# Kernel tuning notes

Hardware: AMD Instinct MI355X
Metric: run time of the kernel (lower is better)

## Reference

```python
import jax, jax.numpy as jnp
import numpy as np

N = 1024      # number of atoms
L = 64        # latent_size
VOCAB = 20    # vocab_size (len(ATOM_CATEGORIES))


def _lin(key, fan_in, fan_out):
    # mimic torch nn.Linear init: U(-1/sqrt(fan_in), 1/sqrt(fan_in))
    kw, kb = jax.random.split(key)
    s = 1.0 / np.sqrt(fan_in)
    W = jax.random.uniform(kw, (fan_in, fan_out), minval=-s, maxval=s, dtype=jnp.float32)
    b = jax.random.uniform(kb, (fan_out,), minval=-s, maxval=s, dtype=jnp.float32)
    return W, b


def setup_inputs() -> dict:
    key = jax.random.key(0)
    ks = jax.random.split(key, 9)
    We1, be1 = _lin(ks[3], 2 * L + 1, L)   # mlp_e layer 1
    We2, be2 = _lin(ks[4], L, L)           # mlp_e layer 2
    Wh1, bh1 = _lin(ks[5], L + 1, L)       # mlp_h layer 1
    Wh2, bh2 = _lin(ks[6], L, L)           # mlp_h layer 2
    Wo, bo = _lin(ks[7], L, 1)             # output_mlp
    return {
        "atom_categories": jax.random.randint(ks[0], (N,), 0, VOCAB),
        "atom_coordinates": jax.random.normal(ks[1], (N, 3), dtype=jnp.float32),
        "learnable_matrix": jax.random.normal(ks[2], (VOCAB, L), dtype=jnp.float32),
        "We1": We1, "be1": be1, "We2": We2, "be2": be2,
        "Wh1": Wh1, "bh1": bh1, "Wh2": Wh2, "bh2": bh2,
        "Wo": Wo, "bo": bo,
    }


def reference(atom_categories, atom_coordinates, learnable_matrix,
              We1, be1, We2, be2, Wh1, bh1, Wh2, bh2, Wo, bo):
    Z = atom_coordinates
    # init_H: learnable_matrix.T @ one_hot(cat) == row gather
    H = learnable_matrix[atom_categories]                       # [N, L]

    # pairwise squared distances ||Z_i - Z_j||^2
    d2 = jnp.sum((Z[:, None, :] - Z[None, :, :]) ** 2, axis=-1)  # [N, N]

    # mlp_e layer 1 on concat(H_i, H_j, d2): split We1 to avoid materializing concat
    W1i, W1j, w1z = We1[:L], We1[L:2 * L], We1[2 * L]            # [L,L],[L,L],[L]
    pre_i = H @ W1i                                              # [N, L]
    pre_j = H @ W1j                                              # [N, L]
    h1 = jnp.tanh(pre_i[:, None, :] + pre_j[None, :, :]
                  + d2[:, :, None] * w1z + be1)                  # [N, N, L]
    W_e = jnp.tanh(h1 @ We2 + be2)                               # [N, N, L]

    # V[i] = sum over j != i of sum_l W_e[i,j,l]
    total = jnp.sum(W_e, axis=(1, 2))                            # [N]
    diag = jnp.einsum('iil->i', W_e)                             # [N]
    V = total - diag                                             # [N]

    # mlp_h on concat(H_i, V_i): split Wh1
    hh = jnp.tanh(H @ Wh1[:L] + V[:, None] * Wh1[L] + bh1)       # [N, L]
    newH = jnp.tanh(hh @ Wh2 + bh2)                              # [N, L]

    Hsum = jnp.sum(newH, axis=0)                                 # [L]
    return (Hsum @ Wo + bo)[0]                                   # scalar
```

## Files before the change

kernel.cpp:

```cpp
#include <hip/hip_runtime.h>
#include <hip/hip_bf16.h>


#define N_ATOMS 1024
#define L_DIM 64
#define TPB 256
#define CSCALE 2.8853900817779268f

typedef _Float16 f16x8 __attribute__((ext_vector_type(8)));
typedef __fp16  fp16x2 __attribute__((ext_vector_type(2)));
typedef float f32x4 __attribute__((ext_vector_type(4)));

__device__ __forceinline__ float tanh_fast(float x) {
    float e = __builtin_amdgcn_exp2f(x * CSCALE);
    float r = __builtin_amdgcn_rcpf(e + 1.0f);
    return fmaf(-2.0f, r, 1.0f);
}

__global__ __launch_bounds__(256) void k_prep(const int* __restrict__ cat,
                                              const float* __restrict__ LM,
                                              const float* __restrict__ We1,
                                              const float* __restrict__ be1,
                                              const float* __restrict__ We2,
                                              const float* __restrict__ be2,
                                              float* __restrict__ H,
                                              float* __restrict__ preI,
                                              float* __restrict__ P3,
                                              f16x8* __restrict__ BHi,
                                              f16x8* __restrict__ BLo,
                                              float* __restrict__ biasPk,
                                              float* __restrict__ out) {
    int t = threadIdx.x;
    int sub = t >> 6, l = t & 63;
    if (blockIdx.x == 0 && t == 0) out[0] = 0.f;

    __shared__ float W1s[2 * L_DIM * L_DIM];
    __shared__ float hs[4][L_DIM];
#pragma unroll
    for (int p = 0; p < 2 * L_DIM * L_DIM / 256; p++)
        W1s[p * 256 + t] = We1[p * 256 + t];

    if (blockIdx.x == 0) {
        int lane = t & 63, grp = t >> 6;
        int nlo = lane & 15, quad = lane >> 4;
#pragma unroll
        for (int pp = grp * 2; pp < grp * 2 + 2; pp++) {
            int nt = pp >> 1, kt = pp & 1;
            f16x8 hi8, lo8;
#pragma unroll
            for (int e = 0; e < 8; e++) {
                float x = We2[(kt * 32 + quad * 8 + e) * L_DIM + nt * 16 + nlo];
                float wp = -2.0f * CSCALE * x;
                _Float16 hi = (_Float16)wp;
                hi8[e] = hi;
                lo8[e] = (_Float16)(wp - (float)hi);
            }
            BHi[pp * 64 + lane] = hi8;
            BLo[pp * 64 + lane] = lo8;
        }
        if (t < 64) {
            float cs = 0.f;
            for (int m = 0; m < L_DIM; m++) cs += We2[m * L_DIM + t];
            biasPk[t] = CSCALE * (be2[t] + cs);
        }
    }

    float bl = be1[l];
    for (int g = 0; g < 4; g++) {
        int i = blockIdx.x * 16 + g * 4 + sub;
        __syncthreads();
        float hv = LM[cat[i] * L_DIM + l];
        hs[sub][l] = hv;
        H[i * L_DIM + l] = hv;
        __syncthreads();
        float s1 = 0.f, s2 = 0.f;
#pragma unroll
        for (int m = 0; m < L_DIM; m++) {
            float h = hs[sub][m];
            s1 = fmaf(h, W1s[m * L_DIM + l], s1);
            s2 = fmaf(h, W1s[(L_DIM + m) * L_DIM + l], s2);
        }
        preI[i * L_DIM + l] = s1 * CSCALE;
        int cc = i >> 4;
        int Ll = i & 15;
        int quad = (l >> 3) & 3;
        int L = quad * 16 + Ll;
        int gg = ((l >> 5) << 1) | ((l >> 2) & 1);
        int e2 = l & 3;
        P3[cc * 1024 + gg * 256 + L * 4 + e2] = (s2 + bl) * CSCALE;
    }
}

__global__ __launch_bounds__(TPB) void k_main(const float* __restrict__ Z,
                                              const float* __restrict__ We1,
                                              const float* __restrict__ preI,
                                              const float* __restrict__ P3,
                                              const f16x8* __restrict__ BHi,
                                              const f16x8* __restrict__ BLo,
                                              const float* __restrict__ biasPk,
                                              float* __restrict__ Vpart) {
    int b = blockIdx.x;
    int i = b >> 1;
    int half = b & 1;
    int t = threadIdx.x;
    int lane = t & 63;
    int wave = t >> 6;
    int nlo = lane & 15;
    int quad = lane >> 4;

    __shared__ float d2s[512];
    __shared__ float red[TPB];
    __shared__ f16x8 bHs[8 * 64];
    __shared__ f16x8 bLs[8 * 64];

    float zi0 = Z[i * 3], zi1 = Z[i * 3 + 1], zi2 = Z[i * 3 + 2];
    for (int p = t; p < 512; p += TPB) {
        int j = half * 512 + p;
        float a = zi0 - Z[j * 3], bb = zi1 - Z[j * 3 + 1], c = zi2 - Z[j * 3 + 2];
        d2s[p] = a * a + bb * bb + c * c;
    }

    if (wave == 0) {
#pragma unroll
        for (int pp = 0; pp < 8; pp++) bHs[pp * 64 + lane] = BHi[pp * 64 + lane];
    } else if (wave == 1) {
#pragma unroll
        for (int pp = 0; pp < 8; pp++) bLs[pp * 64 + lane] = BLo[pp * 64 + lane];
    }

    f32x4 aiR[4], wzR[4];
#pragma unroll
    for (int g = 0; g < 4; g++) {
        int mb = ((g >> 1) << 5) + (quad << 3) + ((g & 1) << 2);
        aiR[g] = *(const f32x4*)(preI + i * L_DIM + mb);
        f32x4 wz = *(const f32x4*)(We1 + 2 * L_DIM * L_DIM + mb);
        wzR[g] = wz * CSCALE;
    }
    float biasR[4];
#pragma unroll
    for (int nt = 0; nt < 4; nt++) biasR[nt] = biasPk[nt * 16 + nlo];

    const float* Pbase = P3 + (half * 32 + wave * 8) * 1024 + lane * 4;

    __syncthreads();

    float Vr = 0.f;
    for (int k = 0; k < 8; k++) {
        int jl0 = (wave * 8 + k) * 16;
        float d2 = d2s[jl0 + nlo];
        const float* pb = Pbase + k * 1024;
        f32x4 p0 = *(const f32x4*)(pb + 0 * 256);
        f32x4 p1 = *(const f32x4*)(pb + 1 * 256);
        f32x4 p2 = *(const f32x4*)(pb + 2 * 256);
        f32x4 p3 = *(const f32x4*)(pb + 3 * 256);

        float h[4][4];
#pragma unroll
        for (int e2 = 0; e2 < 4; e2++) {
            {
                float z = fmaf(d2, wzR[0][e2], aiR[0][e2] + p0[e2]);
                h[0][e2] = __builtin_amdgcn_rcpf(__builtin_amdgcn_exp2f(z) + 1.0f);
            }
            {
                float z = fmaf(d2, wzR[1][e2], aiR[1][e2] + p1[e2]);
                h[1][e2] = __builtin_amdgcn_rcpf(__builtin_amdgcn_exp2f(z) + 1.0f);
            }
            {
                float z = fmaf(d2, wzR[2][e2], aiR[2][e2] + p2[e2]);
                h[2][e2] = __builtin_amdgcn_rcpf(__builtin_amdgcn_exp2f(z) + 1.0f);
            }
            {
                float z = fmaf(d2, wzR[3][e2], aiR[3][e2] + p3[e2]);
                h[3][e2] = __builtin_amdgcn_rcpf(__builtin_amdgcn_exp2f(z) + 1.0f);
            }
        }
        union { f16x8 v; fp16x2 h2[4]; } u0, u1;
        u0.h2[0] = __builtin_amdgcn_cvt_pkrtz(h[0][0], h[0][1]);
        u0.h2[1] = __builtin_amdgcn_cvt_pkrtz(h[0][2], h[0][3]);
        u0.h2[2] = __builtin_amdgcn_cvt_pkrtz(h[1][0], h[1][1]);
        u0.h2[3] = __builtin_amdgcn_cvt_pkrtz(h[1][2], h[1][3]);
        u1.h2[0] = __builtin_amdgcn_cvt_pkrtz(h[2][0], h[2][1]);
        u1.h2[1] = __builtin_amdgcn_cvt_pkrtz(h[2][2], h[2][3]);
        u1.h2[2] = __builtin_amdgcn_cvt_pkrtz(h[3][0], h[3][1]);
        u1.h2[3] = __builtin_amdgcn_cvt_pkrtz(h[3][2], h[3][3]);
        f16x8 aH0 = u0.v, aH1 = u1.v;

#pragma unroll
        for (int nt = 0; nt < 4; nt++) {
            f16x8 bh0 = bHs[(nt * 2 + 0) * 64 + lane];
            f16x8 bh1 = bHs[(nt * 2 + 1) * 64 + lane];
            f16x8 bl0 = bLs[(nt * 2 + 0) * 64 + lane];
            f16x8 bl1 = bLs[(nt * 2 + 1) * 64 + lane];
            f32x4 acc = {biasR[nt], biasR[nt], biasR[nt], biasR[nt]};
            acc = __builtin_amdgcn_mfma_f32_16x16x32_f16(aH0, bh0, acc, 0, 0, 0);
            acc = __builtin_amdgcn_mfma_f32_16x16x32_f16(aH0, bl0, acc, 0, 0, 0);
            acc = __builtin_amdgcn_mfma_f32_16x16x32_f16(aH1, bh1, acc, 0, 0, 0);
            acc = __builtin_amdgcn_mfma_f32_16x16x32_f16(aH1, bl1, acc, 0, 0, 0);
#pragma unroll
            for (int r4 = 0; r4 < 4; r4++) {
                float e = __builtin_amdgcn_exp2f(acc[r4]);
                Vr += __builtin_amdgcn_rcpf(e + 1.0f);
            }
        }
    }

    red[t] = Vr;
    __syncthreads();
    if (t < 64) {
        float r = red[t] + red[t + 64] + red[t + 128] + red[t + 192];
#pragma unroll
        for (int o = 32; o > 0; o >>= 1) r += __shfl_xor(r, o);
        if (t == 0) Vpart[b] = r;
    }
}

__global__ __launch_bounds__(256) void k_post(const float* __restrict__ Vpart,
                                              const float* __restrict__ preI,
                                              const float* __restrict__ P3,
                                              const float* __restrict__ We2,
                                              const float* __restrict__ be2,
                                              const float* __restrict__ H,
                                              const float* __restrict__ Wh1,
                                              const float* __restrict__ bh1,
                                              const float* __restrict__ Wh2,
                                              const float* __restrict__ bh2,
                                              const float* __restrict__ Wo,
                                              const float* __restrict__ bo,
                                              float* __restrict__ out) {
    int t = threadIdx.x;
    int sub = t >> 6, l = t & 63;
    int i = blockIdx.x * 4 + sub;
    __shared__ float hrow[4][L_DIM];
    __shared__ float hh[4][L_DIM];
    __shared__ float dgt[4][L_DIM];

    int cc = i >> 4, Ll = i & 15;
    int q2 = (l >> 3) & 3;
    int g = ((l >> 5) << 1) | ((l >> 2) & 1);
    float z = preI[i * L_DIM + l] + P3[cc * 1024 + g * 256 + (q2 * 16 + Ll) * 4 + (l & 3)];
    float rr = __builtin_amdgcn_rcpf(__builtin_amdgcn_exp2f(z) + 1.0f);
    dgt[sub][l] = fmaf(-2.0f, rr, 1.0f);
    hrow[sub][l] = H[i * L_DIM + l];
    __syncthreads();

    float S = be2[l];
#pragma unroll
    for (int m = 0; m < L_DIM; m++) S = fmaf(dgt[sub][m], We2[m * L_DIM + l], S);
    float rd = __builtin_amdgcn_rcpf(__builtin_amdgcn_exp2f(S * CSCALE) + 1.0f);
#pragma unroll
    for (int o = 32; o > 0; o >>= 1) rd += __shfl_xor(rd, o);

    float Rall = Vpart[2 * i] + Vpart[2 * i + 1];
    float V = fmaf(-2.0f, Rall - rd, (float)(1023 * L_DIM));

    float s = 0.f;
#pragma unroll
    for (int m = 0; m < L_DIM; m++) s = fmaf(hrow[sub][m], Wh1[m * L_DIM + l], s);
    s = fmaf(V, Wh1[L_DIM * L_DIM + l], s) + bh1[l];
    hh[sub][l] = tanh_fast(s);
    __syncthreads();

    float s2 = 0.f;
#pragma unroll
    for (int m = 0; m < L_DIM; m++) s2 = fmaf(hh[sub][m], Wh2[m * L_DIM + l], s2);
    float nh = tanh_fast(s2 + bh2[l]);
    float w = nh * Wo[l];
#pragma unroll
    for (int o = 32; o > 0; o >>= 1) w += __shfl_down(w, o);
    if (l == 0) atomicAdd(out, w + (i == 0 ? bo[0] : 0.f));
}

extern "C" void kernel_launch(void* const* d_in, const int* in_sizes, int n_in,
                              void* d_out, int out_size, void* d_ws, size_t ws_size,
                              hipStream_t stream) {
    const int*   cat = (const int*)  d_in[0];
    const float* Z   = (const float*)d_in[1];
    const float* LM  = (const float*)d_in[2];
    const float* We1 = (const float*)d_in[3];
    const float* be1 = (const float*)d_in[4];
    const float* We2 = (const float*)d_in[5];
    const float* be2 = (const float*)d_in[6];
    const float* Wh1 = (const float*)d_in[7];
    const float* bh1 = (const float*)d_in[8];
    const float* Wh2 = (const float*)d_in[9];
    const float* bh2 = (const float*)d_in[10];
    const float* Wo  = (const float*)d_in[11];
    const float* bo  = (const float*)d_in[12];
    float* out = (float*)d_out;

    float* ws     = (float*)d_ws;
    float* H      = ws;
    float* preI   = H      + N_ATOMS * L_DIM;
    float* P3     = preI   + N_ATOMS * L_DIM;
    float* Vpart  = P3     + N_ATOMS * L_DIM;
    float* BHi_f  = Vpart  + 2 * N_ATOMS;
    float* BLo_f  = BHi_f  + 2048;
    float* biasPk = BLo_f  + 2048;
    f16x8* BHi = (f16x8*)BHi_f;
    f16x8* BLo = (f16x8*)BLo_f;

    k_prep<<<N_ATOMS / 16, 256, 0, stream>>>(cat, LM, We1, be1, We2, be2,
                                             H, preI, P3, BHi, BLo, biasPk, out);
    k_main<<<2 * N_ATOMS, TPB, 0, stream>>>(Z, We1, preI, P3, BHi, BLo, biasPk, Vpart);
    k_post<<<N_ATOMS / 4, 256, 0, stream>>>(Vpart, preI, P3, We2, be2, H,
                                            Wh1, bh1, Wh2, bh2, Wo, bo, out);
}
```

Baseline: 140.6 us.

## Fuse post-processing into main kernel via last-block counter and stage per-atom vectors in LDS

Drops the separate k_post launch. Each atom's two half-blocks bump an atomic counter after writing their partial V, and the block that arrives second runs the mlp_h/output tail for that atom. The per-atom preI and w1z vectors are moved from per-thread registers into shared memory, double-buffered by loop parity, and the k loop is kept rolled, which should cut register pressure. The cost is an extra atomic and threadfence per block plus a serial single-wave tail on the finishing block.

```diff
diff --git a/kernel.cpp b/kernel.cpp
--- a/kernel.cpp
+++ b/kernel.cpp
@@ -29,10 +29,12 @@
                                               f16x8* __restrict__ BHi,
                                               f16x8* __restrict__ BLo,
                                               float* __restrict__ biasPk,
+                                              int* __restrict__ cnt,
                                               float* __restrict__ out) {
     int t = threadIdx.x;
     int sub = t >> 6, l = t & 63;
     if (blockIdx.x == 0 && t == 0) out[0] = 0.f;
+    if (t < 16) cnt[blockIdx.x * 16 + t] = 0;
 
     __shared__ float W1s[2 * L_DIM * L_DIM];
     __shared__ float hs[4][L_DIM];
@@ -98,7 +100,18 @@
                                               const f16x8* __restrict__ BHi,
                                               const f16x8* __restrict__ BLo,
                                               const float* __restrict__ biasPk,
-                                              float* __restrict__ Vpart) {
+                                              float* __restrict__ Vpart,
+                                              int* __restrict__ cnt,
+                                              const float* __restrict__ H,
+                                              const float* __restrict__ We2,
+                                              const float* __restrict__ be2,
+                                              const float* __restrict__ Wh1,
+                                              const float* __restrict__ bh1,
+                                              const float* __restrict__ Wh2,
+                                              const float* __restrict__ bh2,
+                                              const float* __restrict__ Wo,
+                                              const float* __restrict__ bo,
+                                              float* __restrict__ out) {
     int b = blockIdx.x;
     int i = b >> 1;
     int half = b & 1;
@@ -112,6 +125,11 @@
     __shared__ float red[TPB];
     __shared__ f16x8 bHs[8 * 64];
     __shared__ f16x8 bLs[8 * 64];
+    __shared__ f32x4 awAi[2][16];
+    __shared__ f32x4 awWz[2][16];
+    __shared__ float dgt[L_DIM], hrowS[L_DIM], hhS[L_DIM];
+    __shared__ float RallS;
+    __shared__ int finFlag;
 
     float zi0 = Z[i * 3], zi1 = Z[i * 3 + 1], zi2 = Z[i * 3 + 2];
     for (int p = t; p < 512; p += TPB) {
@@ -126,16 +144,20 @@
     } else if (wave == 1) {
 #pragma unroll
         for (int pp = 0; pp < 8; pp++) bLs[pp * 64 + lane] = BLo[pp * 64 + lane];
-    }
-
-    f32x4 aiR[4], wzR[4];
-#pragma unroll
-    for (int g = 0; g < 4; g++) {
-        int mb = ((g >> 1) << 5) + (quad << 3) + ((g & 1) << 2);
-        aiR[g] = *(const f32x4*)(preI + i * L_DIM + mb);
-        f32x4 wz = *(const f32x4*)(We1 + 2 * L_DIM * L_DIM + mb);
-        wzR[g] = wz * CSCALE;
-    }
+    } else if (wave == 2 && lane < 32) {
+        int idx = lane & 15;
+        int g = idx >> 2, q = idx & 3;
+        int mb = ((g >> 1) << 5) + (q << 3) + ((g & 1) << 2);
+        if (lane < 16) {
+            f32x4 v = *(const f32x4*)(preI + i * L_DIM + mb);
+            awAi[0][idx] = v; awAi[1][idx] = v;
+        } else {
+            f32x4 w = *(const f32x4*)(We1 + 2 * L_DIM * L_DIM + mb);
+            w = w * CSCALE;
+            awWz[0][idx] = w; awWz[1][idx] = w;
+        }
+    }
+
     float biasR[4];
 #pragma unroll
     for (int nt = 0; nt < 4; nt++) biasR[nt] = biasPk[nt * 16 + nlo];
@@ -145,45 +167,27 @@
     __syncthreads();
 
     float Vr = 0.f;
+#pragma unroll 1
     for (int k = 0; k < 8; k++) {
+        int par = k & 1;
         int jl0 = (wave * 8 + k) * 16;
         float d2 = d2s[jl0 + nlo];
         const float* pb = Pbase + k * 1024;
-        f32x4 p0 = *(const f32x4*)(pb + 0 * 256);
-        f32x4 p1 = *(const f32x4*)(pb + 1 * 256);
-        f32x4 p2 = *(const f32x4*)(pb + 2 * 256);
-        f32x4 p3 = *(const f32x4*)(pb + 3 * 256);
-
-        float h[4][4];
-#pragma unroll
-        for (int e2 = 0; e2 < 4; e2++) {
-            {
-                float z = fmaf(d2, wzR[0][e2], aiR[0][e2] + p0[e2]);
-                h[0][e2] = __builtin_amdgcn_rcpf(__builtin_amdgcn_exp2f(z) + 1.0f);
-            }
-            {
-                float z = fmaf(d2, wzR[1][e2], aiR[1][e2] + p1[e2]);
-                h[1][e2] = __builtin_amdgcn_rcpf(__builtin_amdgcn_exp2f(z) + 1.0f);
-            }
-            {
-                float z = fmaf(d2, wzR[2][e2], aiR[2][e2] + p2[e2]);
-                h[2][e2] = __builtin_amdgcn_rcpf(__builtin_amdgcn_exp2f(z) + 1.0f);
-            }
-            {
-                float z = fmaf(d2, wzR[3][e2], aiR[3][e2] + p3[e2]);
-                h[3][e2] = __builtin_amdgcn_rcpf(__builtin_amdgcn_exp2f(z) + 1.0f);
-            }
-        }
-        union { f16x8 v; fp16x2 h2[4]; } u0, u1;
-        u0.h2[0] = __builtin_amdgcn_cvt_pkrtz(h[0][0], h[0][1]);
-        u0.h2[1] = __builtin_amdgcn_cvt_pkrtz(h[0][2], h[0][3]);
-        u0.h2[2] = __builtin_amdgcn_cvt_pkrtz(h[1][0], h[1][1]);
-        u0.h2[3] = __builtin_amdgcn_cvt_pkrtz(h[1][2], h[1][3]);
-        u1.h2[0] = __builtin_amdgcn_cvt_pkrtz(h[2][0], h[2][1]);
-        u1.h2[1] = __builtin_amdgcn_cvt_pkrtz(h[2][2], h[2][3]);
-        u1.h2[2] = __builtin_amdgcn_cvt_pkrtz(h[3][0], h[3][1]);
-        u1.h2[3] = __builtin_amdgcn_cvt_pkrtz(h[3][2], h[3][3]);
-        f16x8 aH0 = u0.v, aH1 = u1.v;
+
+        union { f16x8 v; fp16x2 h2[4]; } uu[2];
+#pragma unroll
+        for (int g = 0; g < 4; g++) {
+            f32x4 pg = *(const f32x4*)(pb + g * 256);
+            f32x4 ag = awAi[par][g * 4 + quad];
+            f32x4 wg = awWz[par][g * 4 + quad];
+            float h0 = __builtin_amdgcn_rcpf(__builtin_amdgcn_exp2f(fmaf(d2, wg[0], ag[0] + pg[0])) + 1.0f);
+            float h1 = __builtin_amdgcn_rcpf(__builtin_amdgcn_exp2f(fmaf(d2, wg[1], ag[1] + pg[1])) + 1.0f);
+            float h2 = __builtin_amdgcn_rcpf(__builtin_amdgcn_exp2f(fmaf(d2, wg[2], ag[2] + pg[2])) + 1.0f);
+            float h3 = __builtin_amdgcn_rcpf(__builtin_amdgcn_exp2f(fmaf(d2, wg[3], ag[3] + pg[3])) + 1.0f);
+            uu[g >> 1].h2[(g & 1) * 2 + 0] = __builtin_amdgcn_cvt_pkrtz(h0, h1);
+            uu[g >> 1].h2[(g & 1) * 2 + 1] = __builtin_amdgcn_cvt_pkrtz(h2, h3);
+        }
+        f16x8 aH0 = uu[0].v, aH1 = uu[1].v;
 
 #pragma unroll
         for (int nt = 0; nt < 4; nt++) {
@@ -210,64 +214,57 @@
         float r = red[t] + red[t + 64] + red[t + 128] + red[t + 192];
 #pragma unroll
         for (int o = 32; o > 0; o >>= 1) r += __shfl_xor(r, o);
-        if (t == 0) Vpart[b] = r;
-    }
-}
-
-__global__ __launch_bounds__(256) void k_post(const float* __restrict__ Vpart,
-                                              const float* __restrict__ preI,
-                                              const float* __restrict__ P3,
-                                              const float* __restrict__ We2,
-                                              const float* __restrict__ be2,
-                                              const float* __restrict__ H,
-                                              const float* __restrict__ Wh1,
-                                              const float* __restrict__ bh1,
-                                              const float* __restrict__ Wh2,
-                                              const float* __restrict__ bh2,
-                                              const float* __restrict__ Wo,
-                                              const float* __restrict__ bo,
-                                              float* __restrict__ out) {
-    int t = threadIdx.x;
-    int sub = t >> 6, l = t & 63;
-    int i = blockIdx.x * 4 + sub;
-    __shared__ float hrow[4][L_DIM];
-    __shared__ float hh[4][L_DIM];
-    __shared__ float dgt[4][L_DIM];
-
-    int cc = i >> 4, Ll = i & 15;
-    int q2 = (l >> 3) & 3;
-    int g = ((l >> 5) << 1) | ((l >> 2) & 1);
-    float z = preI[i * L_DIM + l] + P3[cc * 1024 + g * 256 + (q2 * 16 + Ll) * 4 + (l & 3)];
-    float rr = __builtin_amdgcn_rcpf(__builtin_amdgcn_exp2f(z) + 1.0f);
-    dgt[sub][l] = fmaf(-2.0f, rr, 1.0f);
-    hrow[sub][l] = H[i * L_DIM + l];
+        if (t == 0) {
+            Vpart[b] = r;
+            __threadfence();
+            int old = atomicAdd(&cnt[i], 1);
+            finFlag = (old == 1);
+        }
+    }
     __syncthreads();
 
-    float S = be2[l];
-#pragma unroll
-    for (int m = 0; m < L_DIM; m++) S = fmaf(dgt[sub][m], We2[m * L_DIM + l], S);
-    float rd = __builtin_amdgcn_rcpf(__builtin_amdgcn_exp2f(S * CSCALE) + 1.0f);
-#pragma unroll
-    for (int o = 32; o > 0; o >>= 1) rd += __shfl_xor(rd, o);
-
-    float Rall = Vpart[2 * i] + Vpart[2 * i + 1];
-    float V = fmaf(-2.0f, Rall - rd, (float)(1023 * L_DIM));
-
-    float s = 0.f;
-#pragma unroll
-    for (int m = 0; m < L_DIM; m++) s = fmaf(hrow[sub][m], Wh1[m * L_DIM + l], s);
-    s = fmaf(V, Wh1[L_DIM * L_DIM + l], s) + bh1[l];
-    hh[sub][l] = tanh_fast(s);
-    __syncthreads();
-
-    float s2 = 0.f;
-#pragma unroll
-    for (int m = 0; m < L_DIM; m++) s2 = fmaf(hh[sub][m], Wh2[m * L_DIM + l], s2);
-    float nh = tanh_fast(s2 + bh2[l]);
-    float w = nh * Wo[l];
-#pragma unroll
-    for (int o = 32; o > 0; o >>= 1) w += __shfl_down(w, o);
-    if (l == 0) atomicAdd(out, w + (i == 0 ? bo[0] : 0.f));
+    if (finFlag) {
+        if (t == 0) {
+            float ra = atomicAdd(&Vpart[2 * i], 0.f);
+            float rb = atomicAdd(&Vpart[2 * i + 1], 0.f);
+            RallS = ra + rb;
+        }
+        if (t < 64) {
+            int cc = i >> 4, Ll = i & 15;
+            int q2 = (t >> 3) & 3;
+            int g = ((t >> 5) << 1) | ((t >> 2) & 1);
+            float z = preI[i * L_DIM + t] + P3[cc * 1024 + g * 256 + (q2 * 16 + Ll) * 4 + (t & 3)];
+            float rr = __builtin_amdgcn_rcpf(__builtin_amdgcn_exp2f(z) + 1.0f);
+            dgt[t] = fmaf(-2.0f, rr, 1.0f);
+            hrowS[t] = H[i * L_DIM + t];
+        }
+        __syncthreads();
+        if (t < 64) {
+            float S = be2[t];
+#pragma unroll
+            for (int m = 0; m < L_DIM; m++) S = fmaf(dgt[m], We2[m * L_DIM + t], S);
+            float rd = __builtin_amdgcn_rcpf(__builtin_amdgcn_exp2f(S * CSCALE) + 1.0f);
+#pragma unroll
+            for (int o = 32; o > 0; o >>= 1) rd += __shfl_xor(rd, o);
+            float V = fmaf(-2.0f, RallS - rd, (float)(1023 * L_DIM));
+            float s = 0.f;
+#pragma unroll
+            for (int m = 0; m < L_DIM; m++) s = fmaf(hrowS[m], Wh1[m * L_DIM + t], s);
+            s = fmaf(V, Wh1[L_DIM * L_DIM + t], s) + bh1[t];
+            hhS[t] = tanh_fast(s);
+        }
+        __syncthreads();
+        if (t < 64) {
+            float s2 = 0.f;
+#pragma unroll
+            for (int m = 0; m < L_DIM; m++) s2 = fmaf(hhS[m], Wh2[m * L_DIM + t], s2);
+            float nh = tanh_fast(s2 + bh2[t]);
+            float w = nh * Wo[t];
+#pragma unroll
+            for (int o = 32; o > 0; o >>= 1) w += __shfl_down(w, o);
+            if (t == 0) atomicAdd(out, w + (i == 0 ? bo[0] : 0.f));
+        }
+    }
 }
 
 extern "C" void kernel_launch(void* const* d_in, const int* in_sizes, int n_in,
@@ -296,12 +293,13 @@
     float* BHi_f  = Vpart  + 2 * N_ATOMS;
     float* BLo_f  = BHi_f  + 2048;
     float* biasPk = BLo_f  + 2048;
+    int*   cnt    = (int*)(biasPk + 64);
     f16x8* BHi = (f16x8*)BHi_f;
     f16x8* BLo = (f16x8*)BLo_f;
 
     k_prep<<<N_ATOMS / 16, 256, 0, stream>>>(cat, LM, We1, be1, We2, be2,
-                                             H, preI, P3, BHi, BLo, biasPk, out);
-    k_main<<<2 * N_ATOMS, TPB, 0, stream>>>(Z, We1, preI, P3, BHi, BLo, biasPk, Vpart);
-    k_post<<<N_ATOMS / 4, 256, 0, stream>>>(Vpart, preI, P3, We2, be2, H,
+                                             H, preI, P3, BHi, BLo, biasPk, cnt, out);
+    k_main<<<2 * N_ATOMS, TPB, 0, stream>>>(Z, We1, preI, P3, BHi, BLo, biasPk,
+                                            Vpart, cnt, H, We2, be2,
                                             Wh1, bh1, Wh2, bh2, Wo, bo, out);
 }
```

Result: slower. 165.6 us (+17.8%).
